# Performance work log

Hardware: AMD Instinct MI355X
Metric: run time of the kernel (lower is better)

## Reference

```python
import jax, jax.numpy as jnp
import numpy as np

B, P, S = 16, 32, 128
H, V, O = 256, 50000, 128


def lstm_last(x, valid, Wih, Whh, b):
    """Run an LSTM over time and return hidden state at the last valid step.
    x: [T, N, D], valid: [T, N] bool (True = real token). Masked steps hold state,
    so the final carry equals the output at each sequence's last valid position.
    Gate order follows torch: i, f, g, o."""
    N = x.shape[1]
    h0 = jnp.zeros((N, Whh.shape[1]), x.dtype)
    c0 = jnp.zeros((N, Whh.shape[1]), x.dtype)

    def step(carry, inp):
        h, c = carry
        xt, mt = inp
        g = xt @ Wih.T + h @ Whh.T + b  # [N, 4H]
        i, f, gg, o = jnp.split(g, 4, axis=-1)
        cn = jax.nn.sigmoid(f) * c + jax.nn.sigmoid(i) * jnp.tanh(gg)
        hn = jax.nn.sigmoid(o) * jnp.tanh(cn)
        m = mt[:, None]
        return (jnp.where(m, hn, h), jnp.where(m, cn, c)), None

    (h, c), _ = jax.lax.scan(step, (h0, c0), (x, valid))
    return h


def setup_inputs() -> dict:
    key = jax.random.key(0)
    ks = jax.random.split(key, 16)
    x = jax.random.randint(ks[0], (B, P, S), 0, V)
    # ragged lengths: mask is 0 for valid prefix, 1 for padding (matches eq(0).sum())
    lens = jax.random.randint(ks[1], (B, P), 1, S + 1)
    x_mask = (jnp.arange(S)[None, None, :] >= lens[:, :, None]).astype(jnp.int32)
    sc = 0.05
    emb = jax.random.normal(ks[2], (V, H), jnp.float32) * sc
    # sentence-level bidirectional LSTM (input H)
    Wih0f = jax.random.normal(ks[3], (4 * H, H), jnp.float32) * sc
    Whh0f = jax.random.normal(ks[4], (4 * H, H), jnp.float32) * sc
    b0f = jnp.zeros((4 * H,), jnp.float32)
    Wih0b = jax.random.normal(ks[5], (4 * H, H), jnp.float32) * sc
    Whh0b = jax.random.normal(ks[6], (4 * H, H), jnp.float32) * sc
    b0b = jnp.zeros((4 * H,), jnp.float32)
    # paragraph-level LSTM forward direction (input 2H); only fwd hidden is used (hn[0])
    Wih1 = jax.random.normal(ks[7], (4 * H, 2 * H), jnp.float32) * sc
    Whh1 = jax.random.normal(ks[8], (4 * H, H), jnp.float32) * sc
    b1 = jnp.zeros((4 * H,), jnp.float32)
    Wfc = jax.random.normal(ks[9], (O, H), jnp.float32) * sc
    bfc = jnp.zeros((O,), jnp.float32)
    return dict(x=x, x_mask=x_mask, emb=emb, Wih0f=Wih0f, Whh0f=Whh0f, b0f=b0f,
                Wih0b=Wih0b, Whh0b=Whh0b, b0b=b0b, Wih1=Wih1, Whh1=Whh1, b1=b1,
                Wfc=Wfc, bfc=bfc)


def reference(x, x_mask, emb, Wih0f, Whh0f, b0f, Wih0b, Whh0b, b0b,
              Wih1, Whh1, b1, Wfc, bfc):
    valid = (x_mask == 0)  # [B, P, S]
    e = emb[x]  # [B, P, S, H]
    # flatten all sentences and batch them through one LSTM (ragged via masking)
    xt = e.reshape(B * P, S, H).transpose(1, 0, 2)        # [S, B*P, H]
    vt = valid.reshape(B * P, S).T                        # [S, B*P]
    h_f = lstm_last(xt, vt, Wih0f, Whh0f, b0f)            # fwd output at last valid step
    h_b = lstm_last(xt[::-1], vt[::-1], Wih0b, Whh0b, b0b)  # bwd output at t=0
    sen_rep = jnp.concatenate([h_f, h_b], axis=-1).reshape(B, P, 2 * H)
    # paragraph LSTM over sentence representations; take final fwd hidden (hn[0])
    pt = sen_rep.transpose(1, 0, 2)                       # [P, B, 2H]
    pv = jnp.ones((P, B), bool)
    para_h = lstm_last(pt, pv, Wih1, Whh1, b1)            # [B, H]
    return para_h @ Wfc.T + bfc                           # [B, O]
```

## Files before the change

### kernel.cpp

```cpp
#include <hip/hip_runtime.h>
#include <hip/hip_bf16.h>

typedef _Float16 f16;
typedef f16 f16x8 __attribute__((ext_vector_type(8)));
typedef f16 f16x4 __attribute__((ext_vector_type(4)));
typedef float f32x4 __attribute__((ext_vector_type(4)));
typedef int i32x4 __attribute__((ext_vector_type(4)));
typedef unsigned long long ull;

#define MFMA16(a,b,c) __builtin_amdgcn_mfma_f32_16x16x32_f16(a,b,c,0,0,0)
#define BCAST(x) __builtin_bit_cast(f16x8, x)

#define SS 128
#define HH 256
#define NSEQ 512

#define WS_E16   (0)
#define WS_W16   (33554432)
#define WS_SEN   (37224448)
#define WS_U1    (37748736)
#define WS_H1    (38797312)
#define WS_LENS  (38813696)
#define WS_NEED  (38815744)

#define OFF_WIH0F 0
#define OFF_WHH0F 262144
#define OFF_WIH0B 524288
#define OFF_WHH0B 786432
#define OFF_WIH1  1048576
#define OFF_WHH1  1572864

__device__ __forceinline__ float fsig(float x){
  float e = __expf(-x);
  return __builtin_amdgcn_rcpf(1.f + e);
}
__device__ __forceinline__ float ftanh(float x){
  x = fminf(fmaxf(x, -15.f), 15.f);
  float e = __expf(2.f * x);
  return (e - 1.f) * __builtin_amdgcn_rcpf(e + 1.f);
}

__device__ __forceinline__ f16x8 ld_h8(const f16* p){
  union { ull u[2]; f16x8 v; } x;
  x.u[0] = __hip_atomic_load((const ull*)p,       __ATOMIC_RELAXED, __HIP_MEMORY_SCOPE_AGENT);
  x.u[1] = __hip_atomic_load((const ull*)(p + 4), __ATOMIC_RELAXED, __HIP_MEMORY_SCOPE_AGENT);
  return x.v;
}
__device__ __forceinline__ void st_h8b(f16* p, ull v){
  __hip_atomic_store((ull*)p, v, __ATOMIC_RELAXED, __HIP_MEMORY_SCOPE_AGENT);
}

__global__ __launch_bounds__(256) void cvt_all_kernel(
    const float* __restrict__ a, const float* __restrict__ b,
    const float* __restrict__ c, const float* __restrict__ d,
    const float* __restrict__ e, const float* __restrict__ f,
    f16* __restrict__ dst){
  const int i = blockIdx.x * 256 + threadIdx.x;
  const float* s; int off;
  if      (i < 65536)  { s = a; off = i; }
  else if (i < 131072) { s = b; off = i - 65536; }
  else if (i < 196608) { s = c; off = i - 131072; }
  else if (i < 262144) { s = d; off = i - 196608; }
  else if (i < 393216) { s = e; off = i - 262144; }
  else                 { s = f; off = i - 393216; }
  const float4 v = *(const float4*)(s + (size_t)off * 4);
  f16x4 o; o[0] = (f16)v.x; o[1] = (f16)v.y; o[2] = (f16)v.z; o[3] = (f16)v.w;
  *(f16x4*)(dst + (size_t)i * 4) = o;
}

__global__ __launch_bounds__(256) void gather_kernel(const int* __restrict__ x,
                                                     const float* __restrict__ emb,
                                                     f16* __restrict__ e16){
  const int tid = threadIdx.x;
  const int row = blockIdx.x * 4 + (tid >> 6);
  const int l = tid & 63;
  const int t = row >> 9, s = row & 511;
  const int token = x[s * SS + t];
  const float4 v = *(const float4*)(emb + (size_t)token * HH + l * 4);
  f16x4 o; o[0] = (f16)v.x; o[1] = (f16)v.y; o[2] = (f16)v.z; o[3] = (f16)v.w;
  *(f16x4*)(e16 + (size_t)row * HH + l * 4) = o;
}

__global__ __launch_bounds__(64) void lens_kernel(const int* __restrict__ xm,
                                                  int* __restrict__ lens){
  const int s = blockIdx.x, l = threadIdx.x;
  const int v0 = (xm[s * SS + l] == 0) ? 1 : 0;
  const int v1 = (xm[s * SS + 64 + l] == 0) ? 1 : 0;
  unsigned long long b0 = __ballot(v0), b1 = __ballot(v1);
  if (l == 0) lens[s] = __popcll(b0) + __popcll(b1);
}

__global__ __launch_bounds__(256, 1) void lstm0_kernel(
    const f16* __restrict__ e16, const f16* __restrict__ w16,
    const float* __restrict__ b0f, const float* __restrict__ b0b,
    const int* __restrict__ lens, f16* __restrict__ hg,
    unsigned int* __restrict__ cnt, f16* __restrict__ sen16)
{
  __shared__ f16 sbuf[16][72];
  const int tid = threadIdx.x;
  const int w = tid >> 6, l = tid & 63;
  const int lrow = l & 15, lgrp = l >> 4;
  const int bid = blockIdx.x;
  const int xcd = bid & 7, slot = bid >> 3;
  const int grp = xcd * 8 + (slot >> 2);
  const int q = slot & 3;
  const int dir = grp >> 5, sbase = (grp & 31) * 16;
  const int dsbase = dir * 512 + sbase;
  const int jglob = q * 64 + w * 16 + lrow;

  const f16* __restrict__ Wih = w16 + (dir ? OFF_WIH0B : OFF_WIH0F);
  const f16* __restrict__ Whh = w16 + (dir ? OFF_WHH0B : OFF_WHH0F);
  const float* __restrict__ bias = dir ? b0b : b0f;

  i32x4 B[4][16];
  #pragma unroll
  for (int g = 0; g < 4; ++g){
    const int grow = g * 256 + jglob;
    const f16* ph = Whh + (size_t)grow * HH + lgrp * 8;
    const f16* pi = Wih + (size_t)grow * HH + lgrp * 8;
    #pragma unroll
    for (int kk = 0; kk < 8; ++kk){
      B[g][kk]     = *(const i32x4*)(ph + kk * 32);
      B[g][kk + 8] = *(const i32x4*)(pi + kk * 32);
    }
  }
  #pragma unroll
  for (int g = 0; g < 4; ++g)
    #pragma unroll
    for (int kk = 0; kk < 16; ++kk)
      asm volatile("" : "+v"(B[g][kk]));

  float bv[4];
  #pragma unroll
  for (int g = 0; g < 4; ++g) bv[g] = bias[g * 256 + jglob];
  int len4[4];
  #pragma unroll
  for (int r = 0; r < 4; ++r) len4[r] = lens[sbase + lgrp * 4 + r];

  float c4[4] = {}, h4[4] = {};
  unsigned int* cp = cnt + grp * 32;
  const int srow = tid >> 4, part = tid & 15;

  for (int tt = 0; tt < SS; ++tt){
    const int t = dir ? (SS - 1 - tt) : tt;
    const int cb = tt & 1, nb = cb ^ 1;

    f16x8 A[16];
    const f16* ep = e16 + ((size_t)(t * NSEQ + sbase + lrow)) * HH + lgrp * 8;
    #pragma unroll
    for (int kk = 0; kk < 8; ++kk) A[kk + 8] = *(const f16x8*)(ep + kk * 32);

    if (tt > 0){
      if (tid == 0){
        const unsigned int need = 4u * (unsigned)tt;
        while (__hip_atomic_load(cp, __ATOMIC_RELAXED, __HIP_MEMORY_SCOPE_AGENT) < need)
          __builtin_amdgcn_s_sleep(1);
      }
      __syncthreads();
    }

    const f16* hrow = hg + ((size_t)cb * 1024 + dsbase + lrow) * HH + lgrp * 8;
    #pragma unroll
    for (int kk = 0; kk < 8; ++kk) A[kk] = ld_h8(hrow + kk * 32);

    f32x4 ac[4];
    #pragma unroll
    for (int g = 0; g < 4; ++g){ ac[g][0]=0.f; ac[g][1]=0.f; ac[g][2]=0.f; ac[g][3]=0.f; }
    #pragma unroll
    for (int kk = 0; kk < 16; ++kk){
      ac[0] = MFMA16(A[kk], BCAST(B[0][kk]), ac[0]);
      ac[1] = MFMA16(A[kk], BCAST(B[1][kk]), ac[1]);
      ac[2] = MFMA16(A[kk], BCAST(B[2][kk]), ac[2]);
      ac[3] = MFMA16(A[kk], BCAST(B[3][kk]), ac[3]);
    }

    #pragma unroll
    for (int r = 0; r < 4; ++r){
      const float iv = fsig (ac[0][r] + bv[0]);
      const float fv = fsig (ac[1][r] + bv[1]);
      const float gv = ftanh(ac[2][r] + bv[2]);
      const float ov = fsig (ac[3][r] + bv[3]);
      const float cn = fv * c4[r] + iv * gv;
      const float hn = ov * ftanh(cn);
      const bool vld = (t < len4[r]);
      c4[r] = vld ? cn : c4[r];
      h4[r] = vld ? hn : h4[r];
      sbuf[lgrp * 4 + r][w * 16 + lrow] = (f16)h4[r];
    }
    __syncthreads();

    const ull ov = *(const ull*)&sbuf[srow][part * 4];
    st_h8b(hg + ((size_t)nb * 1024 + dsbase + srow) * HH + q * 64 + part * 4, ov);
    __syncthreads();
    if (tid == 0)
      __hip_atomic_fetch_add(cp, 1u, __ATOMIC_RELAXED, __HIP_MEMORY_SCOPE_AGENT);
  }

  #pragma unroll
  for (int r = 0; r < 4; ++r){
    const int s = sbase + lgrp * 4 + r;
    sen16[(size_t)((s & 31) * 16 + (s >> 5)) * 512 + dir * 256 + jglob] = (f16)h4[r];
  }
}

__global__ __launch_bounds__(256, 2) void u1_gemm_kernel(
    const f16* __restrict__ sen16, const f16* __restrict__ w16, f16* __restrict__ U1)
{
  const int tid = threadIdx.x;
  const int w = tid >> 6, l = tid & 63, lrow = l & 15, lgrp = l >> 4;
  const int p = blockIdx.x;
  const f16* __restrict__ Wih1 = w16 + OFF_WIH1;

  f16x8 A[16];
  #pragma unroll
  for (int kb = 0; kb < 16; ++kb)
    A[kb] = *(const f16x8*)&sen16[(size_t)(p * 16 + lrow) * 512 + kb * 32 + lgrp * 8];

  for (int tile = 0; tile < 16; ++tile){
    const int col = (w * 16 + tile) * 16 + lrow;
    const f16* wp = Wih1 + (size_t)col * 512 + lgrp * 8;
    f32x4 acc = {0.f,0.f,0.f,0.f};
    #pragma unroll
    for (int kb = 0; kb < 16; ++kb){
      f16x8 bfrag = *(const f16x8*)(wp + kb * 32);
      acc = MFMA16(A[kb], bfrag, acc);
    }
    f16x4 o4;
    #pragma unroll
    for (int r = 0; r < 4; ++r) o4[r] = (f16)acc[r];
    *(f16x4*)&U1[((size_t)p * 1024 + col) * 16 + lgrp * 4] = o4;
  }
}

__global__ __launch_bounds__(256, 1) void lstm1_kernel(
    const f16* __restrict__ w16, const f16* __restrict__ U1,
    const float* __restrict__ b1, f16* __restrict__ hg2,
    unsigned int* __restrict__ cnt2, float* __restrict__ h1)
{
  const int bid = blockIdx.x;
  if (bid & 7) return;
  __shared__ f16 sbuf[16][72];
  const int q = bid >> 3;
  const int tid = threadIdx.x;
  const int w = tid >> 6, l = tid & 63;
  const int lrow = l & 15, lgrp = l >> 4;
  const int jglob = q * 64 + w * 16 + lrow;
  const f16* __restrict__ Whh = w16 + OFF_WHH1;

  i32x4 B[4][8];
  #pragma unroll
  for (int g = 0; g < 4; ++g){
    const f16* ph = Whh + (size_t)(g * 256 + jglob) * HH + lgrp * 8;
    #pragma unroll
    for (int kk = 0; kk < 8; ++kk) B[g][kk] = *(const i32x4*)(ph + kk * 32);
  }
  #pragma unroll
  for (int g = 0; g < 4; ++g)
    #pragma unroll
    for (int kk = 0; kk < 8; ++kk)
      asm volatile("" : "+v"(B[g][kk]));

  float bv[4];
  #pragma unroll
  for (int g = 0; g < 4; ++g) bv[g] = b1[g * 256 + jglob];
  float c4[4] = {}, h4[4] = {};
  const int srow = tid >> 4, part = tid & 15;

  for (int pt = 0; pt < 32; ++pt){
    const int cb = pt & 1, nb = cb ^ 1;

    f16x4 u[4];
    #pragma unroll
    for (int g = 0; g < 4; ++g)
      u[g] = *(const f16x4*)&U1[((size_t)pt * 1024 + g * 256 + jglob) * 16 + lgrp * 4];

    if (pt > 0){
      if (tid == 0){
        const unsigned int need = 4u * (unsigned)pt;
        while (__hip_atomic_load(cnt2, __ATOMIC_RELAXED, __HIP_MEMORY_SCOPE_AGENT) < need)
          __builtin_amdgcn_s_sleep(1);
      }
      __syncthreads();
    }

    f16x8 A[8];
    const f16* hrow = hg2 + ((size_t)cb * 16 + lrow) * HH + lgrp * 8;
    #pragma unroll
    for (int kk = 0; kk < 8; ++kk) A[kk] = ld_h8(hrow + kk * 32);

    f32x4 ac[4];
    #pragma unroll
    for (int g = 0; g < 4; ++g){ ac[g][0]=0.f; ac[g][1]=0.f; ac[g][2]=0.f; ac[g][3]=0.f; }
    #pragma unroll
    for (int kk = 0; kk < 8; ++kk){
      ac[0] = MFMA16(A[kk], BCAST(B[0][kk]), ac[0]);
      ac[1] = MFMA16(A[kk], BCAST(B[1][kk]), ac[1]);
      ac[2] = MFMA16(A[kk], BCAST(B[2][kk]), ac[2]);
      ac[3] = MFMA16(A[kk], BCAST(B[3][kk]), ac[3]);
    }

    #pragma unroll
    for (int r = 0; r < 4; ++r){
      const float iv = fsig (ac[0][r] + (float)u[0][r] + bv[0]);
      const float fv = fsig (ac[1][r] + (float)u[1][r] + bv[1]);
      const float gv = ftanh(ac[2][r] + (float)u[2][r] + bv[2]);
      const float ov = fsig (ac[3][r] + (float)u[3][r] + bv[3]);
      const float cn = fv * c4[r] + iv * gv;
      c4[r] = cn;
      h4[r] = ov * ftanh(cn);
      sbuf[lgrp * 4 + r][w * 16 + lrow] = (f16)h4[r];
    }
    __syncthreads();

    const ull ov = *(const ull*)&sbuf[srow][part * 4];
    st_h8b(hg2 + ((size_t)nb * 16 + srow) * HH + q * 64 + part * 4, ov);
    __syncthreads();
    if (tid == 0)
      __hip_atomic_fetch_add(cnt2, 1u, __ATOMIC_RELAXED, __HIP_MEMORY_SCOPE_AGENT);
  }

  #pragma unroll
  for (int r = 0; r < 4; ++r)
    h1[(lgrp * 4 + r) * 256 + jglob] = h4[r];
}

__global__ __launch_bounds__(256) void fc_kernel(const float* __restrict__ h1,
                                                 const float* __restrict__ Wfc,
                                                 const float* __restrict__ bfc,
                                                 float* __restrict__ out){
  __shared__ float hl[16 * 256];
  const int tid = threadIdx.x;
  for (int i = tid; i < 4096; i += 256) hl[i] = h1[i];
  __syncthreads();
  const int o = tid & 127, half = tid >> 7;
  float acc[8];
  #pragma unroll
  for (int i = 0; i < 8; ++i) acc[i] = bfc[o];
  const float* wp = Wfc + (size_t)o * 256;
  for (int j = 0; j < 256; ++j){
    const float wv = wp[j];
    #pragma unroll
    for (int i = 0; i < 8; ++i) acc[i] += wv * hl[(half * 8 + i) * 256 + j];
  }
  #pragma unroll
  for (int i = 0; i < 8; ++i) out[(half * 8 + i) * 128 + o] = acc[i];
}

extern "C" void kernel_launch(void* const* d_in, const int* in_sizes, int n_in,
                              void* d_out, int out_size, void* d_ws, size_t ws_size,
                              hipStream_t stream) {
  if (ws_size < (size_t)WS_NEED) return;

  const int*   x     = (const int*)  d_in[0];
  const int*   xm    = (const int*)  d_in[1];
  const float* emb   = (const float*)d_in[2];
  const float* Wih0f = (const float*)d_in[3];
  const float* Whh0f = (const float*)d_in[4];
  const float* b0f   = (const float*)d_in[5];
  const float* Wih0b = (const float*)d_in[6];
  const float* Whh0b = (const float*)d_in[7];
  const float* b0b   = (const float*)d_in[8];
  const float* Wih1  = (const float*)d_in[9];
  const float* Whh1  = (const float*)d_in[10];
  const float* b1    = (const float*)d_in[11];
  const float* Wfc   = (const float*)d_in[12];
  const float* bfc   = (const float*)d_in[13];
  float* out = (float*)d_out;
  char*  ws  = (char*)d_ws;

  f16*   e16   = (f16*)(ws + WS_E16);
  f16*   w16   = (f16*)(ws + WS_W16);
  f16*   sen16 = (f16*)(ws + WS_SEN);
  f16*   U1    = (f16*)(ws + WS_U1);
  float* h1    = (float*)(ws + WS_H1);
  int*   lens  = (int*)(ws + WS_LENS);
  f16*          hg0  = (f16*)(ws + WS_U1);
  unsigned int* cnt0 = (unsigned int*)(ws + WS_H1);
  f16*          hg2  = (f16*)(ws + 0);
  unsigned int* cnt2 = (unsigned int*)(ws + 16384);

  cvt_all_kernel<<<1792, 256, 0, stream>>>(Wih0f, Whh0f, Wih0b, Whh0b, Wih1, Whh1, w16);
  gather_kernel<<<16384, 256, 0, stream>>>(x, emb, e16);
  lens_kernel<<<512, 64, 0, stream>>>(xm, lens);

  hipMemsetAsync(ws + WS_U1, 0, 524288, stream);
  hipMemsetAsync(ws + WS_H1, 0, 8192, stream);
  lstm0_kernel<<<256, 256, 0, stream>>>(e16, w16, b0f, b0b, lens, hg0, cnt0, sen16);

  hipMemsetAsync(ws + 0, 0, 16512, stream);
  u1_gemm_kernel<<<32, 256, 0, stream>>>(sen16, w16, U1);
  lstm1_kernel<<<32, 256, 0, stream>>>(w16, U1, b1, hg2, cnt2, h1);
  fc_kernel<<<1, 256, 0, stream>>>(h1, Wfc, bfc, out);
}
```

Baseline: 832.9 us.

## Replace counter barriers with tagged data exchange and fuse embedding gather into LSTM

Cross-block hidden-state exchange no longer uses a shared atomic counter followed by separate data loads. Each 64-bit store now packs three f16 hidden values plus a 16-bit step tag, and consumers poll their own words until the tag matches, then assemble the state in LDS. The gather kernel and its large intermediate buffer are removed: tokens are staged in LDS and embedding rows are read and converted inside the recurrent loop. The paragraph LSTM is also regrouped from four blocks to two, each computing 128 hidden units. The trade-off is many polling threads, extra LDS traffic and reliance on the 0xFF memset as an initial tag sentinel.

```diff
diff --git a/kernel.cpp b/kernel.cpp
--- a/kernel.cpp
+++ b/kernel.cpp
@@ -7,6 +7,7 @@
 typedef float f32x4 __attribute__((ext_vector_type(4)));
 typedef int i32x4 __attribute__((ext_vector_type(4)));
 typedef unsigned long long ull;
+typedef unsigned short u16;
 
 #define MFMA16(a,b,c) __builtin_amdgcn_mfma_f32_16x16x32_f16(a,b,c,0,0,0)
 #define BCAST(x) __builtin_bit_cast(f16x8, x)
@@ -15,7 +16,8 @@
 #define HH 256
 #define NSEQ 512
 
-#define WS_E16   (0)
+#define WS_TAGS0 (0)
+#define WS_TAGS1 (1572864)
 #define WS_W16   (33554432)
 #define WS_SEN   (37224448)
 #define WS_U1    (37748736)
@@ -38,16 +40,6 @@
   x = fminf(fmaxf(x, -15.f), 15.f);
   float e = __expf(2.f * x);
   return (e - 1.f) * __builtin_amdgcn_rcpf(e + 1.f);
-}
-
-__device__ __forceinline__ f16x8 ld_h8(const f16* p){
-  union { ull u[2]; f16x8 v; } x;
-  x.u[0] = __hip_atomic_load((const ull*)p,       __ATOMIC_RELAXED, __HIP_MEMORY_SCOPE_AGENT);
-  x.u[1] = __hip_atomic_load((const ull*)(p + 4), __ATOMIC_RELAXED, __HIP_MEMORY_SCOPE_AGENT);
-  return x.v;
-}
-__device__ __forceinline__ void st_h8b(f16* p, ull v){
-  __hip_atomic_store((ull*)p, v, __ATOMIC_RELAXED, __HIP_MEMORY_SCOPE_AGENT);
 }
 
 __global__ __launch_bounds__(256) void cvt_all_kernel(
@@ -68,19 +60,6 @@
   *(f16x4*)(dst + (size_t)i * 4) = o;
 }
 
-__global__ __launch_bounds__(256) void gather_kernel(const int* __restrict__ x,
-                                                     const float* __restrict__ emb,
-                                                     f16* __restrict__ e16){
-  const int tid = threadIdx.x;
-  const int row = blockIdx.x * 4 + (tid >> 6);
-  const int l = tid & 63;
-  const int t = row >> 9, s = row & 511;
-  const int token = x[s * SS + t];
-  const float4 v = *(const float4*)(emb + (size_t)token * HH + l * 4);
-  f16x4 o; o[0] = (f16)v.x; o[1] = (f16)v.y; o[2] = (f16)v.z; o[3] = (f16)v.w;
-  *(f16x4*)(e16 + (size_t)row * HH + l * 4) = o;
-}
-
 __global__ __launch_bounds__(64) void lens_kernel(const int* __restrict__ xm,
                                                   int* __restrict__ lens){
   const int s = blockIdx.x, l = threadIdx.x;
@@ -91,21 +70,22 @@
 }
 
 __global__ __launch_bounds__(256, 1) void lstm0_kernel(
-    const f16* __restrict__ e16, const f16* __restrict__ w16,
+    const int* __restrict__ x, const float* __restrict__ emb,
+    const f16* __restrict__ w16,
     const float* __restrict__ b0f, const float* __restrict__ b0b,
-    const int* __restrict__ lens, f16* __restrict__ hg,
-    unsigned int* __restrict__ cnt, f16* __restrict__ sen16)
+    const int* __restrict__ lens, char* __restrict__ tags,
+    f16* __restrict__ sen16)
 {
-  __shared__ f16 sbuf[16][72];
+  __shared__ f16 himg[2][16][264];
+  __shared__ int xlds[16][128];
   const int tid = threadIdx.x;
   const int w = tid >> 6, l = tid & 63;
   const int lrow = l & 15, lgrp = l >> 4;
   const int bid = blockIdx.x;
-  const int xcd = bid & 7, slot = bid >> 3;
-  const int grp = xcd * 8 + (slot >> 2);
-  const int q = slot & 3;
+  const int xcd = bid & 7, slot8 = bid >> 3;
+  const int grp = xcd * 8 + (slot8 >> 2);
+  const int q = slot8 & 3;
   const int dir = grp >> 5, sbase = (grp & 31) * 16;
-  const int dsbase = dir * 512 + sbase;
   const int jglob = q * 64 + w * 16 + lrow;
 
   const f16* __restrict__ Wih = w16 + (dir ? OFF_WIH0B : OFF_WIH0F);
@@ -137,31 +117,81 @@
   #pragma unroll
   for (int r = 0; r < 4; ++r) len4[r] = lens[sbase + lgrp * 4 + r];
 
+  for (int i = tid; i < 2 * 16 * 264; i += 256) ((f16*)himg)[i] = (f16)0.f;
+  for (int i = tid; i < 2048; i += 256)
+    ((int*)xlds)[i] = x[(sbase + (i >> 7)) * SS + (i & 127)];
+  __syncthreads();
+
+  const int nu = (tid < 32) ? 5 : 4;
+  int uoff[5], urow[5], uj0[5], ujb[5];
+  #pragma unroll
+  for (int i = 0; i < 5; ++i){
+    int u = tid + (i << 8); if (u > 1055) u = 1055;
+    const int qi = u / 352;
+    const int rem = u - qi * 352;
+    const int r = rem / 22;
+    const int wd = rem - r * 22;
+    const int qa = qi + (qi >= q ? 1 : 0);
+    uoff[i] = ((((r << 2) + qa) * 22 + wd) << 3);
+    urow[i] = r; ujb[i] = wd * 3; uj0[i] = (qa << 6) + wd * 3;
+  }
+  const int prow = tid >> 4, pw = tid & 15;
+  char* const gbase = tags + (size_t)grp * 22528;
+
   float c4[4] = {}, h4[4] = {};
-  unsigned int* cp = cnt + grp * 32;
-  const int srow = tid >> 4, part = tid & 15;
 
   for (int tt = 0; tt < SS; ++tt){
     const int t = dir ? (SS - 1 - tt) : tt;
-    const int cb = tt & 1, nb = cb ^ 1;
-
+    const int cs = tt & 1, ps = cs ^ 1;
+
+    const int tk = xlds[lrow][t];
     f16x8 A[16];
-    const f16* ep = e16 + ((size_t)(t * NSEQ + sbase + lrow)) * HH + lgrp * 8;
-    #pragma unroll
-    for (int kk = 0; kk < 8; ++kk) A[kk + 8] = *(const f16x8*)(ep + kk * 32);
+    #pragma unroll
+    for (int kk = 0; kk < 8; ++kk){
+      const float* ep = emb + (size_t)tk * HH + kk * 32 + lgrp * 8;
+      const float4 u0 = *(const float4*)ep;
+      const float4 u1 = *(const float4*)(ep + 4);
+      f16x8 v;
+      v[0]=(f16)u0.x; v[1]=(f16)u0.y; v[2]=(f16)u0.z; v[3]=(f16)u0.w;
+      v[4]=(f16)u1.x; v[5]=(f16)u1.y; v[6]=(f16)u1.z; v[7]=(f16)u1.w;
+      A[kk + 8] = v;
+    }
 
     if (tt > 0){
-      if (tid == 0){
-        const unsigned int need = 4u * (unsigned)tt;
-        while (__hip_atomic_load(cp, __ATOMIC_RELAXED, __HIP_MEMORY_SCOPE_AGENT) < need)
-          __builtin_amdgcn_s_sleep(1);
+      const u16 need = (u16)(tt - 1);
+      const char* bb = gbase + (size_t)ps * 11264;
+      ull vv[5] = {0,0,0,0,0};
+      bool gt[5] = {false,false,false,false,false};
+      int rem = nu;
+      while (rem > 0){
+        ull tmp[5];
+        #pragma unroll
+        for (int i = 0; i < 5; ++i)
+          if (i < nu && !gt[i])
+            tmp[i] = __hip_atomic_load((const ull*)(bb + uoff[i]),
+                                       __ATOMIC_RELAXED, __HIP_MEMORY_SCOPE_AGENT);
+        #pragma unroll
+        for (int i = 0; i < 5; ++i)
+          if (i < nu && !gt[i] && (u16)(tmp[i] >> 48) == need){
+            vv[i] = tmp[i]; gt[i] = true; --rem;
+          }
+        if (rem > 0) __builtin_amdgcn_s_sleep(1);
       }
-      __syncthreads();
-    }
-
-    const f16* hrow = hg + ((size_t)cb * 1024 + dsbase + lrow) * HH + lgrp * 8;
-    #pragma unroll
-    for (int kk = 0; kk < 8; ++kk) A[kk] = ld_h8(hrow + kk * 32);
+      #pragma unroll
+      for (int i = 0; i < 5; ++i)
+        if (i < nu){
+          #pragma unroll
+          for (int c = 0; c < 3; ++c)
+            if (ujb[i] + c < 64)
+              himg[ps][urow[i]][uj0[i] + c] =
+                __builtin_bit_cast(f16, (u16)(vv[i] >> (16 * c)));
+        }
+    }
+    __syncthreads();
+
+    #pragma unroll
+    for (int kk = 0; kk < 8; ++kk)
+      A[kk] = *(const f16x8*)&himg[ps][lrow][kk * 32 + lgrp * 8];
 
     f32x4 ac[4];
     #pragma unroll
@@ -185,15 +215,21 @@
       const bool vld = (t < len4[r]);
       c4[r] = vld ? cn : c4[r];
       h4[r] = vld ? hn : h4[r];
-      sbuf[lgrp * 4 + r][w * 16 + lrow] = (f16)h4[r];
+      himg[cs][lgrp * 4 + r][jglob] = (f16)h4[r];
     }
     __syncthreads();
 
-    const ull ov = *(const ull*)&sbuf[srow][part * 4];
-    st_h8b(hg + ((size_t)nb * 1024 + dsbase + srow) * HH + q * 64 + part * 4, ov);
-    __syncthreads();
-    if (tid == 0)
-      __hip_atomic_fetch_add(cp, 1u, __ATOMIC_RELAXED, __HIP_MEMORY_SCOPE_AGENT);
+    char* const ob = gbase + (size_t)cs * 11264;
+    #pragma unroll 2
+    for (int wd = pw; wd < 22; wd += 16){
+      const int j0 = wd * 3;
+      const u16 a0 = __builtin_bit_cast(u16, himg[cs][prow][(q << 6) + j0]);
+      const u16 a1 = (j0 + 1 < 64) ? __builtin_bit_cast(u16, himg[cs][prow][(q << 6) + j0 + 1]) : (u16)0;
+      const u16 a2 = (j0 + 2 < 64) ? __builtin_bit_cast(u16, himg[cs][prow][(q << 6) + j0 + 2]) : (u16)0;
+      const ull wv = (ull)a0 | ((ull)a1 << 16) | ((ull)a2 << 32) | ((ull)(u16)tt << 48);
+      __hip_atomic_store((ull*)(ob + ((((prow << 2) + q) * 22 + wd) << 3)), wv,
+                         __ATOMIC_RELAXED, __HIP_MEMORY_SCOPE_AGENT);
+    }
   }
 
   #pragma unroll
@@ -234,94 +270,155 @@
 
 __global__ __launch_bounds__(256, 1) void lstm1_kernel(
     const f16* __restrict__ w16, const f16* __restrict__ U1,
-    const float* __restrict__ b1, f16* __restrict__ hg2,
-    unsigned int* __restrict__ cnt2, float* __restrict__ h1)
+    const float* __restrict__ b1, char* __restrict__ tags,
+    float* __restrict__ h1)
 {
   const int bid = blockIdx.x;
   if (bid & 7) return;
-  __shared__ f16 sbuf[16][72];
-  const int q = bid >> 3;
+  const int m = bid >> 3;
+  __shared__ f16 himg[2][16][264];
   const int tid = threadIdx.x;
   const int w = tid >> 6, l = tid & 63;
   const int lrow = l & 15, lgrp = l >> 4;
-  const int jglob = q * 64 + w * 16 + lrow;
   const f16* __restrict__ Whh = w16 + OFF_WHH1;
 
-  i32x4 B[4][8];
-  #pragma unroll
-  for (int g = 0; g < 4; ++g){
-    const f16* ph = Whh + (size_t)(g * 256 + jglob) * HH + lgrp * 8;
-    #pragma unroll
-    for (int kk = 0; kk < 8; ++kk) B[g][kk] = *(const i32x4*)(ph + kk * 32);
-  }
+  int jg[2];
+  jg[0] = m * 128 + w * 32 + lrow;
+  jg[1] = jg[0] + 16;
+
+  i32x4 B[4][2][8];
   #pragma unroll
   for (int g = 0; g < 4; ++g)
     #pragma unroll
+    for (int p = 0; p < 2; ++p){
+      const f16* ph = Whh + (size_t)(g * 256 + jg[p]) * HH + lgrp * 8;
+      #pragma unroll
+      for (int kk = 0; kk < 8; ++kk) B[g][p][kk] = *(const i32x4*)(ph + kk * 32);
+    }
+  #pragma unroll
+  for (int g = 0; g < 4; ++g)
+    #pragma unroll
+    for (int p = 0; p < 2; ++p)
+      #pragma unroll
+      for (int kk = 0; kk < 8; ++kk)
+        asm volatile("" : "+v"(B[g][p][kk]));
+
+  float bv[4][2];
+  #pragma unroll
+  for (int g = 0; g < 4; ++g)
+    #pragma unroll
+    for (int p = 0; p < 2; ++p) bv[g][p] = b1[g * 256 + jg[p]];
+
+  for (int i = tid; i < 2 * 16 * 264; i += 256) ((f16*)himg)[i] = (f16)0.f;
+  __syncthreads();
+
+  const int nu = (tid < 176) ? 3 : 2;
+  int uoff[3], urow[3], uj0[3], ujb[3];
+  #pragma unroll
+  for (int i = 0; i < 3; ++i){
+    int u = tid + (i << 8); if (u > 687) u = 687;
+    const int r = u / 43;
+    const int wd = u - r * 43;
+    uoff[i] = ((((r << 1) + (1 - m)) * 43 + wd) << 3);
+    urow[i] = r; ujb[i] = wd * 3; uj0[i] = (1 - m) * 128 + wd * 3;
+  }
+  const int prow = tid >> 4, pw = tid & 15;
+
+  float c4[2][4] = {}, h4[2][4] = {};
+
+  for (int pt = 0; pt < 32; ++pt){
+    const int cs = pt & 1, ps = cs ^ 1;
+
+    f16x4 u[4][2];
+    #pragma unroll
+    for (int g = 0; g < 4; ++g)
+      #pragma unroll
+      for (int p = 0; p < 2; ++p)
+        u[g][p] = *(const f16x4*)&U1[((size_t)pt * 1024 + g * 256 + jg[p]) * 16 + lgrp * 4];
+
+    if (pt > 0){
+      const u16 need = (u16)(pt - 1);
+      const char* bb = tags + (size_t)ps * 11008;
+      ull vv[3] = {0,0,0};
+      bool gt[3] = {false,false,false};
+      int rem = nu;
+      while (rem > 0){
+        ull tmp[3];
+        #pragma unroll
+        for (int i = 0; i < 3; ++i)
+          if (i < nu && !gt[i])
+            tmp[i] = __hip_atomic_load((const ull*)(bb + uoff[i]),
+                                       __ATOMIC_RELAXED, __HIP_MEMORY_SCOPE_AGENT);
+        #pragma unroll
+        for (int i = 0; i < 3; ++i)
+          if (i < nu && !gt[i] && (u16)(tmp[i] >> 48) == need){
+            vv[i] = tmp[i]; gt[i] = true; --rem;
+          }
+        if (rem > 0) __builtin_amdgcn_s_sleep(1);
+      }
+      #pragma unroll
+      for (int i = 0; i < 3; ++i)
+        if (i < nu){
+          #pragma unroll
+          for (int c = 0; c < 3; ++c)
+            if (ujb[i] + c < 128)
+              himg[ps][urow[i]][uj0[i] + c] =
+                __builtin_bit_cast(f16, (u16)(vv[i] >> (16 * c)));
+        }
+    }
+    __syncthreads();
+
+    f16x8 A[8];
+    #pragma unroll
     for (int kk = 0; kk < 8; ++kk)
-      asm volatile("" : "+v"(B[g][kk]));
-
-  float bv[4];
-  #pragma unroll
-  for (int g = 0; g < 4; ++g) bv[g] = b1[g * 256 + jglob];
-  float c4[4] = {}, h4[4] = {};
-  const int srow = tid >> 4, part = tid & 15;
-
-  for (int pt = 0; pt < 32; ++pt){
-    const int cb = pt & 1, nb = cb ^ 1;
-
-    f16x4 u[4];
+      A[kk] = *(const f16x8*)&himg[ps][lrow][kk * 32 + lgrp * 8];
+
+    f32x4 ac[4][2];
     #pragma unroll
     for (int g = 0; g < 4; ++g)
-      u[g] = *(const f16x4*)&U1[((size_t)pt * 1024 + g * 256 + jglob) * 16 + lgrp * 4];
-
-    if (pt > 0){
-      if (tid == 0){
-        const unsigned int need = 4u * (unsigned)pt;
-        while (__hip_atomic_load(cnt2, __ATOMIC_RELAXED, __HIP_MEMORY_SCOPE_AGENT) < need)
-          __builtin_amdgcn_s_sleep(1);
+      #pragma unroll
+      for (int p = 0; p < 2; ++p){ ac[g][p][0]=0.f; ac[g][p][1]=0.f; ac[g][p][2]=0.f; ac[g][p][3]=0.f; }
+    #pragma unroll
+    for (int kk = 0; kk < 8; ++kk)
+      #pragma unroll
+      for (int g = 0; g < 4; ++g){
+        ac[g][0] = MFMA16(A[kk], BCAST(B[g][0][kk]), ac[g][0]);
+        ac[g][1] = MFMA16(A[kk], BCAST(B[g][1][kk]), ac[g][1]);
       }
-      __syncthreads();
-    }
-
-    f16x8 A[8];
-    const f16* hrow = hg2 + ((size_t)cb * 16 + lrow) * HH + lgrp * 8;
-    #pragma unroll
-    for (int kk = 0; kk < 8; ++kk) A[kk] = ld_h8(hrow + kk * 32);
-
-    f32x4 ac[4];
-    #pragma unroll
-    for (int g = 0; g < 4; ++g){ ac[g][0]=0.f; ac[g][1]=0.f; ac[g][2]=0.f; ac[g][3]=0.f; }
-    #pragma unroll
-    for (int kk = 0; kk < 8; ++kk){
-      ac[0] = MFMA16(A[kk], BCAST(B[0][kk]), ac[0]);
-      ac[1] = MFMA16(A[kk], BCAST(B[1][kk]), ac[1]);
-      ac[2] = MFMA16(A[kk], BCAST(B[2][kk]), ac[2]);
-      ac[3] = MFMA16(A[kk], BCAST(B[3][kk]), ac[3]);
-    }
-
-    #pragma unroll
-    for (int r = 0; r < 4; ++r){
-      const float iv = fsig (ac[0][r] + (float)u[0][r] + bv[0]);
-      const float fv = fsig (ac[1][r] + (float)u[1][r] + bv[1]);
-      const float gv = ftanh(ac[2][r] + (float)u[2][r] + bv[2]);
-      const float ov = fsig (ac[3][r] + (float)u[3][r] + bv[3]);
-      const float cn = fv * c4[r] + iv * gv;
-      c4[r] = cn;
-      h4[r] = ov * ftanh(cn);
-      sbuf[lgrp * 4 + r][w * 16 + lrow] = (f16)h4[r];
-    }
+
+    #pragma unroll
+    for (int p = 0; p < 2; ++p)
+      #pragma unroll
+      for (int r = 0; r < 4; ++r){
+        const float iv = fsig (ac[0][p][r] + (float)u[0][p][r] + bv[0][p]);
+        const float fv = fsig (ac[1][p][r] + (float)u[1][p][r] + bv[1][p]);
+        const float gv = ftanh(ac[2][p][r] + (float)u[2][p][r] + bv[2][p]);
+        const float ov = fsig (ac[3][p][r] + (float)u[3][p][r] + bv[3][p]);
+        const float cn = fv * c4[p][r] + iv * gv;
+        c4[p][r] = cn;
+        h4[p][r] = ov * ftanh(cn);
+        himg[cs][lgrp * 4 + r][jg[p]] = (f16)h4[p][r];
+      }
     __syncthreads();
 
-    const ull ov = *(const ull*)&sbuf[srow][part * 4];
-    st_h8b(hg2 + ((size_t)nb * 16 + srow) * HH + q * 64 + part * 4, ov);
-    __syncthreads();
-    if (tid == 0)
-      __hip_atomic_fetch_add(cnt2, 1u, __ATOMIC_RELAXED, __HIP_MEMORY_SCOPE_AGENT);
-  }
-
-  #pragma unroll
-  for (int r = 0; r < 4; ++r)
-    h1[(lgrp * 4 + r) * 256 + jglob] = h4[r];
+    char* const ob = tags + (size_t)cs * 11008;
+    #pragma unroll 3
+    for (int wd = pw; wd < 43; wd += 16){
+      const int j0 = wd * 3;
+      const u16 a0 = __builtin_bit_cast(u16, himg[cs][prow][m * 128 + j0]);
+      const u16 a1 = (j0 + 1 < 128) ? __builtin_bit_cast(u16, himg[cs][prow][m * 128 + j0 + 1]) : (u16)0;
+      const u16 a2 = (j0 + 2 < 128) ? __builtin_bit_cast(u16, himg[cs][prow][m * 128 + j0 + 2]) : (u16)0;
+      const ull wv = (ull)a0 | ((ull)a1 << 16) | ((ull)a2 << 32) | ((ull)(u16)pt << 48);
+      __hip_atomic_store((ull*)(ob + ((((prow << 1) + m) * 43 + wd) << 3)), wv,
+                         __ATOMIC_RELAXED, __HIP_MEMORY_SCOPE_AGENT);
+    }
+  }
+
+  #pragma unroll
+  for (int p = 0; p < 2; ++p)
+    #pragma unroll
+    for (int r = 0; r < 4; ++r)
+      h1[(lgrp * 4 + r) * 256 + jg[p]] = h4[p][r];
 }
 
 __global__ __launch_bounds__(256) void fc_kernel(const float* __restrict__ h1,
@@ -368,27 +465,20 @@
   float* out = (float*)d_out;
   char*  ws  = (char*)d_ws;
 
-  f16*   e16   = (f16*)(ws + WS_E16);
   f16*   w16   = (f16*)(ws + WS_W16);
   f16*   sen16 = (f16*)(ws + WS_SEN);
   f16*   U1    = (f16*)(ws + WS_U1);
   float* h1    = (float*)(ws + WS_H1);
   int*   lens  = (int*)(ws + WS_LENS);
-  f16*          hg0  = (f16*)(ws + WS_U1);
-  unsigned int* cnt0 = (unsigned int*)(ws + WS_H1);
-  f16*          hg2  = (f16*)(ws + 0);
-  unsigned int* cnt2 = (unsigned int*)(ws + 16384);
+  char*  tags0 = ws + WS_TAGS0;
+  char*  tags1 = ws + WS_TAGS1;
 
   cvt_all_kernel<<<1792, 256, 0, stream>>>(Wih0f, Whh0f, Wih0b, Whh0b, Wih1, Whh1, w16);
-  gather_kernel<<<16384, 256, 0, stream>>>(x, emb, e16);
   lens_kernel<<<512, 64, 0, stream>>>(xm, lens);
-
-  hipMemsetAsync(ws + WS_U1, 0, 524288, stream);
-  hipMemsetAsync(ws + WS_H1, 0, 8192, stream);
-  lstm0_kernel<<<256, 256, 0, stream>>>(e16, w16, b0f, b0b, lens, hg0, cnt0, sen16);
-
-  hipMemsetAsync(ws + 0, 0, 16512, stream);
+  hipMemsetAsync(ws, 0xFF, 1594880, stream);
+
+  lstm0_kernel<<<256, 256, 0, stream>>>(x, emb, w16, b0f, b0b, lens, tags0, sen16);
   u1_gemm_kernel<<<32, 256, 0, stream>>>(sen16, w16, U1);
-  lstm1_kernel<<<32, 256, 0, stream>>>(w16, U1, b1, hg2, cnt2, h1);
+  lstm1_kernel<<<9, 256, 0, stream>>>(w16, U1, b1, tags1, h1);
   fc_kernel<<<1, 256, 0, stream>>>(h1, Wfc, bfc, out);
 }
```

New measurement: 813.4 us. -2.3%, faster.
